# Kernel optimization log

Hardware: AMD Instinct MI355X
Metric: run time of the kernel (lower is better)

Reference implementation:

```python
import jax, jax.numpy as jnp
import numpy as np
import math
from jax import lax

RNN = 256
N_MELS = 80
RF = 5
FRAME = N_MELS * RF  # 400
DYN_CH = 8
DYN_K = 21
STATIC_CH = 8
STATIC_K = 21
PRIOR_LEN = 11


def _betabinom_pmf(n, a, b):
    k = np.arange(n + 1, dtype=np.float64)
    lg = lambda x: np.array([math.lgamma(float(v)) for v in np.atleast_1d(x)])
    logC = lg(n + 1) - lg(k + 1) - lg(n - k + 1)
    logB = lg(k + a) + lg(n - k + b) - lg(np.full_like(k, n + a + b))
    logB0 = math.lgamma(a) + math.lgamma(b) - math.lgamma(a + b)
    return np.exp(logC + logB - logB0)

# prior buffer, flipped as in the torch module (register_buffer('P', ...flip(0)))
PRIOR = jnp.asarray(_betabinom_pmf(PRIOR_LEN - 1, 0.1, 0.9)[::-1].copy(), dtype=jnp.float32)


def gru_cell(x, h, wi, bi, wh, bh):
    # torch GRUCell math
    gi = x @ wi.T + bi
    gh = h @ wh.T + bh
    ir, iz, i_n = jnp.split(gi, 3, axis=-1)
    hr, hz, h_n = jnp.split(gh, 3, axis=-1)
    r = jax.nn.sigmoid(ir + hr)
    z = jax.nn.sigmoid(iz + hz)
    n = jnp.tanh(i_n + r * h_n)
    return (1.0 - z) * n + z * h


def dca(s, alpha, dW_w, dW_b, dV_w, dF_w, dU_w, dT_w, dT_b, dv_w):
    B, S = alpha.shape
    # betabinomial prior: causal conv with flipped pmf
    ap = jnp.pad(alpha, ((0, 0), (PRIOR_LEN - 1, 0)))[:, None, :]  # [B,1,S+10]
    p = lax.conv_general_dilated(ap, PRIOR.reshape(1, 1, -1), (1,), [(0, 0)],
                                 dimension_numbers=('NCH', 'OIH', 'NCH'))[:, 0]  # [B,S]
    p = jnp.log(jnp.clip(p, 1e-6))
    # dynamic filters: one set of 8 kernels per batch element
    G = jnp.tanh(s @ dW_w.T + dW_b) @ dV_w.T  # [B, 8*21]
    g = lax.conv_general_dilated(alpha[None, :, :], G.reshape(B * DYN_CH, 1, DYN_K),
                                 (1,), [((DYN_K - 1) // 2,) * 2],
                                 dimension_numbers=('NCH', 'OIH', 'NCH'),
                                 feature_group_count=B)  # [1, B*8, S]
    g = g.reshape(B, DYN_CH, S).transpose(0, 2, 1)  # [B,S,8]
    # static filters
    f = lax.conv_general_dilated(alpha[:, None, :], dF_w, (1,), [((STATIC_K - 1) // 2,) * 2],
                                 dimension_numbers=('NCH', 'OIH', 'NCH')).transpose(0, 2, 1)  # [B,S,8]
    e = (jnp.tanh(f @ dU_w.T + g @ dT_w.T + dT_b) @ dv_w.T)[..., 0] + p  # [B,S]
    return jax.nn.softmax(e, axis=-1)


def _decode(encoder_outputs, p1_w, p1_b, p2_w, p2_b, a_wi, a_bi, a_wh, a_bh,
            dW_w, dW_b, dV_w, dF_w, dU_w, dT_w, dT_b, dv_w, l_w, l_b,
            g1_wi, g1_bi, g1_wh, g1_bh, g2_wi, g2_bi, g2_wh, g2_bh, pr_w, pr_b, T_dec):
    B, S, _ = encoder_outputs.shape
    frame0 = jnp.zeros((B, FRAME), jnp.float32)
    alpha0 = jnp.zeros((B, S), jnp.float32).at[:, 0].set(1.0)
    ctx0 = jnp.zeros((B, 3 * RNN), jnp.float32)
    h0 = jnp.zeros((B, RNN), jnp.float32)

    def step(carry, _):
        frame, alpha, ctx, h_att, h1, h2 = carry
        # pre-net (eval mode: dropout is identity)
        pre = jax.nn.relu(jax.nn.relu(frame @ p1_w.T + p1_b) @ p2_w.T + p2_b)  # [B,128]
        h_att = gru_cell(jnp.concatenate([ctx, pre], axis=-1), h_att, a_wi, a_bi, a_wh, a_bh)
        alpha = dca(h_att, alpha, dW_w, dW_b, dV_w, dF_w, dU_w, dT_w, dT_b, dv_w)
        ctx = jnp.einsum('bs,bsd->bd', alpha, encoder_outputs)  # [B,768]
        x = jnp.concatenate([ctx, h_att], axis=-1) @ l_w.T + l_b  # [B,256]
        h1 = gru_cell(x, h1, g1_wi, g1_bi, g1_wh, g1_bh)
        x = x + h1
        h2 = gru_cell(x, h2, g2_wi, g2_bi, g2_wh, g2_bh)
        x = x + h2
        out = x @ pr_w.T + pr_b  # [B,400]
        return (out, alpha, ctx, h_att, h1, h2), out

    (_, alphaT, _, _, _, _), outs = lax.scan(step, (frame0, alpha0, ctx0, h0, h0, h0), None, length=T_dec)
    # outs: [T,B,400] -> [B,80,T*5]
    mel = outs.reshape(T_dec, B, N_MELS, RF).transpose(1, 2, 0, 3).reshape(B, N_MELS, T_dec * RF)
    return mel


def setup_inputs() -> dict:
    key = jax.random.key(0)
    ks = iter(jax.random.split(key, 40))
    w = lambda shape: jax.random.normal(next(ks), shape, jnp.float32) * 0.05
    z = lambda shape: jnp.zeros(shape, jnp.float32)
    B, S, D = 64, 512, 768
    return {
        'encoder_outputs': jax.random.normal(next(ks), (B, S, D), jnp.float32),
        'p1_w': w((RNN, FRAME)), 'p1_b': z((RNN,)),
        'p2_w': w((RNN // 2, RNN)), 'p2_b': z((RNN // 2,)),
        'a_wi': w((3 * RNN, 896)), 'a_bi': z((3 * RNN,)), 'a_wh': w((3 * RNN, RNN)), 'a_bh': z((3 * RNN,)),
        'dW_w': w((128, RNN)), 'dW_b': z((128,)),
        'dV_w': w((DYN_CH * DYN_K, 128)),
        'dF_w': w((STATIC_CH, 1, STATIC_K)),
        'dU_w': w((128, STATIC_CH)),
        'dT_w': w((128, DYN_CH)), 'dT_b': z((128,)),
        'dv_w': w((1, 128)),
        'l_w': w((RNN, 4 * RNN)), 'l_b': z((RNN,)),
        'g1_wi': w((3 * RNN, RNN)), 'g1_bi': z((3 * RNN,)), 'g1_wh': w((3 * RNN, RNN)), 'g1_bh': z((3 * RNN,)),
        'g2_wi': w((3 * RNN, RNN)), 'g2_bi': z((3 * RNN,)), 'g2_wh': w((3 * RNN, RNN)), 'g2_bh': z((3 * RNN,)),
        'pr_w': w((FRAME, RNN)), 'pr_b': z((FRAME,)),
        'T_dec': 250,
    }


def reference(encoder_outputs, p1_w, p1_b, p2_w, p2_b, a_wi, a_bi, a_wh, a_bh,
              dW_w, dW_b, dV_w, dF_w, dU_w, dT_w, dT_b, dv_w, l_w, l_b,
              g1_wi, g1_bi, g1_wh, g1_bh, g2_wi, g2_bi, g2_wh, g2_bh, pr_w, pr_b, T_dec):
    return _decode(encoder_outputs, p1_w, p1_b, p2_w, p2_b, a_wi, a_bi, a_wh, a_bh,
                   dW_w, dW_b, dV_w, dF_w, dU_w, dT_w, dT_b, dv_w, l_w, l_b,
                   g1_wi, g1_bi, g1_wh, g1_bh, g2_wi, g2_bi, g2_wh, g2_bh, pr_w, pr_b, T_dec)
```

## Files before the change

kernel.cpp:

```cpp
#include <hip/hip_runtime.h>
#include <cmath>

#define TDEC 250
#define EPS_A 1e-6f

#define NB_GIC  64
#define NB_GA   128
#define NB_WH1  144
#define NB_WH2  152
#define NBLK    160

#define B_CTX(p)  (8192   + (p)*49152)
#define B_HATT(p) (106496 + (p)*16384)
#define B_H1(p)   (139264 + (p)*16384)
#define B_H2(p)   (172032 + (p)*16384)
#define B_GIC(p)  (204800 + (p)*49152)
#define B_GH(p)   (303104 + (p)*49152)
#define B_GH1(p)  (401408 + (p)*49152)
#define B_GH2(p)  (499712 + (p)*49152)
#define ZERO_END  598016
#define CVT_OFF   598016

#define OP1   0u
#define OP2   106496u
#define OAWI  139264u
#define OAWH  827392u
#define ODW   1024000u
#define ODV   1056768u
#define OLW   1078272u
#define OG1I  1340416u
#define OG2I  1537024u
#define OG1H  1733632u
#define OG2H  1930240u
#define OPR   2126848u

struct Prior { float v[11]; };

struct KArgs {
  const float *enc;
  const float *p1w,*p1b,*p2w,*p2b;
  const float *awi,*abi,*awh,*abh;
  const float *dWw,*dWb,*dVw,*dFw,*dUw,*dTw,*dTb,*dvw;
  const float *lw,*lb;
  const float *g1wi,*g1bi,*g1wh,*g1bh;
  const float *g2wi,*g2bi,*g2wh,*g2bh;
  const float *prw,*prb;
  float* ws; float* dout;
  Prior pr;
};

__device__ __forceinline__ float gld(const float* p) {
  return __uint_as_float(__hip_atomic_load((const unsigned*)p, __ATOMIC_RELAXED, __HIP_MEMORY_SCOPE_AGENT));
}
__device__ __forceinline__ void gst(float* p, float v) {
  __hip_atomic_store((unsigned*)p, __float_as_uint(v), __ATOMIC_RELAXED, __HIP_MEMORY_SCOPE_AGENT);
}
__device__ __forceinline__ float sigm(float x) { return 1.f / (1.f + expf(-x)); }

__device__ __forceinline__ float dot8(uint4 w, float4 x0, float4 x1) {
  float a;
  a = __uint_as_float(w.x << 16) * x0.x;
  a = fmaf(__uint_as_float(w.x & 0xffff0000u), x0.y, a);
  a = fmaf(__uint_as_float(w.y << 16),         x0.z, a);
  a = fmaf(__uint_as_float(w.y & 0xffff0000u), x0.w, a);
  a = fmaf(__uint_as_float(w.z << 16),         x1.x, a);
  a = fmaf(__uint_as_float(w.z & 0xffff0000u), x1.y, a);
  a = fmaf(__uint_as_float(w.w << 16),         x1.z, a);
  a = fmaf(__uint_as_float(w.w & 0xffff0000u), x1.w, a);
  return a;
}

__global__ __launch_bounds__(256) void k_init(float* ws) {
  int idx = blockIdx.x * 256 + threadIdx.x;
  for (int i = idx; i < ZERO_END; i += gridDim.x * 256) ws[i] = 0.f;
}

struct CvtSeg { const float* src; unsigned dst; unsigned n; };
struct CvtArgs { CvtSeg s[12]; };
__global__ __launch_bounds__(256) void k_cvt(CvtArgs c, unsigned short* wb) {
  for (unsigned i = blockIdx.x * 256 + threadIdx.x; i < 256u * 416u; i += gridDim.x * 256) {
    unsigned row = i / 416u, col = i - row * 416u;
    unsigned short v = 0;
    if (col < 400u) {
      unsigned u = __float_as_uint(c.s[0].src[row * 400u + col]);
      v = (unsigned short)((u + 0x7fffu + ((u >> 16) & 1u)) >> 16);
    }
    wb[OP1 + i] = v;
  }
  for (int seg = 1; seg < 12; ++seg) {
    const float* s = c.s[seg].src;
    unsigned short* d = wb + c.s[seg].dst;
    unsigned n = c.s[seg].n;
    for (unsigned i = blockIdx.x * 256 + threadIdx.x; i < n; i += gridDim.x * 256) {
      unsigned u = __float_as_uint(s[i]);
      d[i] = (unsigned short)((u + 0x7fffu + ((u >> 16) & 1u)) >> 16);
    }
  }
}

__device__ __forceinline__ void postw(unsigned* fl, int word, unsigned v) {
  asm volatile("s_waitcnt vmcnt(0)" ::: "memory");
  __syncthreads();
  if (threadIdx.x == 0)
    __hip_atomic_store(&fl[blockIdx.x * 32 + word], v, __ATOMIC_RELAXED, __HIP_MEMORY_SCOPE_AGENT);
}
template <int SLP>
__device__ __forceinline__ void pollge(unsigned* fl, int line, int word, unsigned v) {
  while (__hip_atomic_load(&fl[line * 32 + word], __ATOMIC_RELAXED, __HIP_MEMORY_SCOPE_AGENT) < v)
    __builtin_amdgcn_s_sleep(SLP);
}

__global__ __launch_bounds__(1024, 1) void k_decode(KArgs A) {
  __shared__ __align__(16) float sm[16640];
  float* ws = A.ws;
  unsigned* fl = (unsigned*)ws;
  const unsigned short* wb = (const unsigned short*)(ws + CVT_OFF);
  const int blk = blockIdx.x;
  const int tid = threadIdx.x;

  if (blk < 64) {
    const int b = blk, bg = b >> 4;
    float* alpha = sm;
    float* hattl = sm + 512;
    float* h1l   = sm + 768;
    float* h2l   = sm + 1024;
    float* fr    = sm + 1280;
    float* ctxl  = sm + 1696;
    float* xl    = sm + 2464;
    float* x2l   = sm + 2720;
    float* x3l   = sm + 2976;
    float* sal   = sm + 3232;
    float* h1s   = sm + 3776;
    float* pre   = sm + 4032;
    float* sgi   = sm + 4160;
    float* sgh   = sm + 4928;
    float* t1    = sm + 5696;
    float* Gl    = sm + 5824;
    float* sdF   = sm + 6000;
    float* sdU   = sm + 6176;
    float* sdT   = sm + 7200;
    float* sdtb  = sm + 8224;
    float* sdv   = sm + 8352;
    float* es    = sm + 8480;
    float* e     = sm + 9504;
    float* red   = sm + 10016;
    int*   wc    = (int*)(sm + 10032);
    float* lv    = sm + 10040;
    short* li    = (short*)(sm + 10552);

    if (tid < 512) alpha[tid] = (tid == 0) ? 1.f : 0.f;
    if (tid < 256) { hattl[tid] = 0.f; h1l[tid] = 0.f; h2l[tid] = 0.f; }
    if (tid < 416) fr[tid] = 0.f;
    if (tid < 176) sdF[tid] = (tid < 168) ? A.dFw[tid] : 0.f;
    sdU[tid] = A.dUw[tid];
    sdT[tid] = A.dTw[tid];
    if (tid < 128) { sdtb[tid] = A.dTb[tid]; sdv[tid] = A.dvw[tid]; }
    __syncthreads();

    for (int t = 0; t < TDEC; ++t) {
      const int p = t & 1;
      if (tid < 544) { int sg = tid - 10; sal[tid] = (sg >= 0 && sg < 512) ? alpha[sg] : 0.f; }
      __syncthreads();
      {
        int j = tid >> 2, part = tid & 3;
        const uint4* wr = (const uint4*)(wb + OP1 + (size_t)j * 416) + part * 13;
        const float4* xr = (const float4*)fr + part * 26;
        float a = 0.f;
#pragma unroll
        for (int k4 = 0; k4 < 13; ++k4) a += dot8(wr[k4], xr[2*k4], xr[2*k4+1]);
        a += __shfl_xor(a, 1); a += __shfl_xor(a, 2);
        if (part == 0) h1s[j] = fmaxf(a + A.p1b[j], 0.f);
      }
      __syncthreads();
      {
        int j = tid >> 3, part = tid & 7;
        const uint4* wr = (const uint4*)(wb + OP2 + (size_t)j * 256) + part * 4;
        const float4* xr = (const float4*)h1s + part * 8;
        float a = 0.f;
#pragma unroll
        for (int k4 = 0; k4 < 4; ++k4) a += dot8(wr[k4], xr[2*k4], xr[2*k4+1]);
        a += __shfl_xor(a, 1); a += __shfl_xor(a, 2); a += __shfl_xor(a, 4);
        if (part == 0) pre[j] = fmaxf(a + A.p2b[j], 0.f);
      }
      __syncthreads();
      float gipre = 0.f;
      if (tid < 768) {
        const uint4* wr = (const uint4*)(wb + OAWI + (size_t)tid * 896 + 768);
        const float4* xr = (const float4*)pre;
        float a = 0.f;
#pragma unroll
        for (int k4 = 0; k4 < 16; ++k4) a += dot8(wr[k4], xr[2*k4], xr[2*k4+1]);
        gipre = a;
      } else if (tid < 784) {
        pollge<1>(fl, NB_GIC + bg * 16 + (tid - 768), 0, (unsigned)(t + 1));
      } else if (tid < 788) {
        pollge<1>(fl, NB_GA + bg * 4 + (tid - 784), 0, (unsigned)(t + 1));
      }
      __syncthreads();
      if (tid < 768) {
        sgi[tid] = gipre + gld(ws + B_GIC(p) + b * 768 + tid) + A.abi[tid];
        sgh[tid] = gld(ws + B_GH(p) + b * 768 + tid) + A.abh[tid];
      }
      __syncthreads();
      if (tid < 256) {
        float r = sigm(sgi[tid] + sgh[tid]);
        float z = sigm(sgi[256 + tid] + sgh[256 + tid]);
        float n = tanhf(sgi[512 + tid] + r * sgh[512 + tid]);
        float hnew = (1.f - z) * n + z * hattl[tid];
        hattl[tid] = hnew;
        gst(ws + B_HATT(p) + b * 256 + tid, hnew);
      }
      postw(fl, 1, (unsigned)(t + 1));
      {
        int j = tid >> 3, part = tid & 7;
        const uint4* wr = (const uint4*)(wb + ODW + (size_t)j * 256) + part * 4;
        const float4* xr = (const float4*)hattl + part * 8;
        float a = 0.f;
#pragma unroll
        for (int k4 = 0; k4 < 4; ++k4) a += dot8(wr[k4], xr[2*k4], xr[2*k4+1]);
        a += __shfl_xor(a, 1); a += __shfl_xor(a, 2); a += __shfl_xor(a, 4);
        if (part == 0) t1[j] = tanhf(a + A.dWb[j]);
      }
      __syncthreads();
      if (tid < 168) {
        const uint4* wr = (const uint4*)(wb + ODV + (size_t)tid * 128);
        const float4* xr = (const float4*)t1;
        float a = 0.f;
#pragma unroll
        for (int k4 = 0; k4 < 16; ++k4) a += dot8(wr[k4], xr[2*k4], xr[2*k4+1]);
        Gl[tid] = a;
      }
      __syncthreads();
      {
        int sl = tid >> 1, half = tid & 1;
        float f0[8], g0[8];
#pragma unroll
        for (int q = 0; q < 8; ++q) {
          float fa = 0.f, ga = 0.f;
#pragma unroll
          for (int k = 0; k < 21; ++k) {
            float a = sal[sl + k];
            fa = fmaf(sdF[q * 21 + k], a, fa);
            ga = fmaf(Gl[q * 21 + k], a, ga);
          }
          f0[q] = fa; g0[q] = ga;
        }
        float acc = 0.f;
        for (int cc = half * 64; cc < half * 64 + 64; ++cc) {
          float a = sdtb[cc];
#pragma unroll
          for (int q = 0; q < 8; ++q)
            a = fmaf(sdU[cc * 8 + q], f0[q], fmaf(sdT[cc * 8 + q], g0[q], a));
          acc = fmaf(sdv[cc], tanhf(a), acc);
        }
        es[sl * 2 + half] = acc;
      }
      __syncthreads();
      if (tid < 512) {
        float pr = 0.f;
#pragma unroll
        for (int k = 0; k < 11; ++k) pr = fmaf(A.pr.v[k], sal[tid + k], pr);
        e[tid] = es[tid * 2] + es[tid * 2 + 1] + logf(fmaxf(pr, 1e-6f));
      }
      __syncthreads();
      {
        int lane = tid & 63, wv = tid >> 6;
        float e0 = (tid < 512) ? e[tid] : -1e30f;
        float m = e0;
        for (int o = 32; o; o >>= 1) m = fmaxf(m, __shfl_xor(m, o));
        if (lane == 0) red[wv] = m;
        __syncthreads();
        m = red[0];
        for (int w = 1; w < 8; ++w) m = fmaxf(m, red[w]);
        float p0 = (tid < 512) ? expf(e0 - m) : 0.f;
        float s = p0;
        for (int o = 32; o; o >>= 1) s += __shfl_xor(s, o);
        __syncthreads();
        if (lane == 0) red[wv] = s;
        __syncthreads();
        float tot = red[0];
        for (int w = 1; w < 8; ++w) tot += red[w];
        float inv = 1.f / tot;
        float a0 = p0 * inv;
        if (tid < 512) alpha[tid] = a0;
        unsigned long long mk = __ballot(tid < 512 && a0 > EPS_A);
        if (lane == 0 && wv < 8) wc[wv] = (int)__popcll(mk);
        __syncthreads();
        int base = 0;
        for (int w = 0; w < wv && w < 8; ++w) base += wc[w];
        int n = 0;
        for (int w = 0; w < 8; ++w) n += wc[w];
        unsigned long long below = (1ull << lane) - 1ull;
        if (tid < 512 && a0 > EPS_A) {
          int pp = base + (int)__popcll(mk & below);
          li[pp] = (short)tid; lv[pp] = a0;
        }
        __syncthreads();
        const float* encb = A.enc + (size_t)b * 512 * 768;
        if (tid < 768) {
          float acc = 0.f;
          int i = 0;
          for (; i + 4 <= n; i += 4) {
            float v0 = gld(encb + (size_t)li[i] * 768 + tid);
            float v1 = gld(encb + (size_t)li[i+1] * 768 + tid);
            float v2 = gld(encb + (size_t)li[i+2] * 768 + tid);
            float v3 = gld(encb + (size_t)li[i+3] * 768 + tid);
            acc = fmaf(lv[i],v0, fmaf(lv[i+1],v1, fmaf(lv[i+2],v2, fmaf(lv[i+3],v3, acc))));
          }
          for (; i < n; ++i) acc = fmaf(lv[i], gld(encb + (size_t)li[i] * 768 + tid), acc);
          ctxl[tid] = acc;
          gst(ws + B_CTX(p) + b * 768 + tid, acc);
        }
      }
      postw(fl, 0, (unsigned)(t + 1));
      {
        int j = tid >> 2, part = tid & 3;
        const uint4* wr = (const uint4*)(wb + OLW + (size_t)j * 1024) + part * 32;
        const float4* xr = (part < 3) ? ((const float4*)ctxl + part * 64) : (const float4*)hattl;
        float a = 0.f;
#pragma unroll 16
        for (int k4 = 0; k4 < 32; ++k4) a += dot8(wr[k4], xr[2*k4], xr[2*k4+1]);
        a += __shfl_xor(a, 1); a += __shfl_xor(a, 2);
        if (part == 0) xl[j] = a + A.lb[j];
      }
      __syncthreads();
      {
        float giv = 0.f;
        if (tid < 768) {
          const uint4* wr = (const uint4*)(wb + OG1I + (size_t)tid * 256);
          const float4* xr = (const float4*)xl;
          float a = 0.f;
#pragma unroll 16
          for (int k4 = 0; k4 < 32; ++k4) a += dot8(wr[k4], xr[2*k4], xr[2*k4+1]);
          giv = a;
        } else if (tid < 776) {
          pollge<1>(fl, NB_WH1 + (tid - 768), 0, (unsigned)(t + 1));
        }
        __syncthreads();
        if (tid < 768) {
          sgi[tid] = giv + A.g1bi[tid];
          sgh[tid] = gld(ws + B_GH1(p) + b * 768 + tid);
        }
        __syncthreads();
        if (tid < 256) {
          float r = sigm(sgi[tid] + sgh[tid]);
          float z = sigm(sgi[256 + tid] + sgh[256 + tid]);
          float n = tanhf(sgi[512 + tid] + r * sgh[512 + tid]);
          float hnew = (1.f - z) * n + z * h1l[tid];
          h1l[tid] = hnew;
          gst(ws + B_H1(p) + b * 256 + tid, hnew);
          x2l[tid] = xl[tid] + hnew;
        }
        postw(fl, 2, (unsigned)(t + 1));
      }
      {
        float giv = 0.f;
        if (tid < 768) {
          const uint4* wr = (const uint4*)(wb + OG2I + (size_t)tid * 256);
          const float4* xr = (const float4*)x2l;
          float a = 0.f;
#pragma unroll 16
          for (int k4 = 0; k4 < 32; ++k4) a += dot8(wr[k4], xr[2*k4], xr[2*k4+1]);
          giv = a;
        } else if (tid < 776) {
          pollge<1>(fl, NB_WH2 + (tid - 768), 0, (unsigned)(t + 1));
        }
        __syncthreads();
        if (tid < 768) {
          sgi[tid] = giv + A.g2bi[tid];
          sgh[tid] = gld(ws + B_GH2(p) + b * 768 + tid);
        }
        __syncthreads();
        if (tid < 256) {
          float r = sigm(sgi[tid] + sgh[tid]);
          float z = sigm(sgi[256 + tid] + sgh[256 + tid]);
          float n = tanhf(sgi[512 + tid] + r * sgh[512 + tid]);
          float hnew = (1.f - z) * n + z * h2l[tid];
          h2l[tid] = hnew;
          gst(ws + B_H2(p) + b * 256 + tid, hnew);
          x3l[tid] = x2l[tid] + hnew;
        }
        postw(fl, 3, (unsigned)(t + 1));
      }
      if (tid < 800) {
        int j = tid >> 1, part = tid & 1;
        const uint4* wr = (const uint4*)(wb + OPR + (size_t)j * 256) + part * 16;
        const float4* xr = (const float4*)x3l + part * 32;
        float a = 0.f;
#pragma unroll 16
        for (int k4 = 0; k4 < 16; ++k4) a += dot8(wr[k4], xr[2*k4], xr[2*k4+1]);
        a += __shfl_xor(a, 1);
        if (part == 0) {
          float v = a + A.prb[j];
          fr[j] = v;
          gst(A.dout + (size_t)b * 100000 + (j / 5) * 1250 + t * 5 + (j % 5), v);
        }
      }
      __syncthreads();
    }
  } else if (blk < NB_GA) {
    int rb = blk - NB_GIC, bg = rb >> 4, jg = rb & 15;
    int B = bg * 16, R0 = jg * 48;
    float* cl = sm;
    for (int t = 0; t < TDEC; ++t) {
      const int p = t & 1;
      if (tid < 16) pollge<4>(fl, bg * 16 + tid, 0, (unsigned)t);
      __syncthreads();
      for (int idx = tid; idx < 12288; idx += 1024) {
        int bb = idx / 768, k = idx - bb * 768;
        cl[bb * 772 + k] = gld(ws + B_CTX(p ^ 1) + (B + bb) * 768 + k);
      }
      __syncthreads();
      if (tid < 768) {
        int rr = tid >> 4, bb = tid & 15;
        int row = R0 + rr;
        const uint4* wr = (const uint4*)(wb + OAWI + (size_t)row * 896);
        const float4* xr = (const float4*)(cl + bb * 772);
        float a = 0.f;
#pragma unroll 16
        for (int k4 = 0; k4 < 96; ++k4) a += dot8(wr[k4], xr[2*k4], xr[2*k4+1]);
        gst(ws + B_GIC(p) + (B + bb) * 768 + row, a);
      }
      postw(fl, 0, (unsigned)(t + 1));
    }
  } else if (blk < NB_WH1) {
    int rb = blk - NB_GA, bg = rb >> 2, jg = rb & 3;
    int B = bg * 16, R0 = jg * 192;
    float* hl = sm;
    for (int t = 0; t < TDEC; ++t) {
      const int p = t & 1;
      if (tid < 16) pollge<4>(fl, bg * 16 + tid, 1, (unsigned)t);
      __syncthreads();
      for (int idx = tid; idx < 4096; idx += 1024) {
        int bb = idx >> 8, k = idx & 255;
        hl[bb * 260 + k] = gld(ws + B_HATT(p ^ 1) + (B + bb) * 256 + k);
      }
      __syncthreads();
#pragma unroll
      for (int pass = 0; pass < 3; ++pass) {
        int rr = pass * 64 + (tid >> 4), bb = tid & 15;
        int row = R0 + rr;
        const uint4* wr = (const uint4*)(wb + OAWH + (size_t)row * 256);
        const float4* xr = (const float4*)(hl + bb * 260);
        float a = 0.f;
#pragma unroll 16
        for (int k4 = 0; k4 < 32; ++k4) a += dot8(wr[k4], xr[2*k4], xr[2*k4+1]);
        gst(ws + B_GH(p) + (B + bb) * 768 + row, a);
      }
      postw(fl, 0, (unsigned)(t + 1));
    }
  } else {
    const int isW2 = (blk >= NB_WH2);
    const int w = blk - (isW2 ? NB_WH2 : NB_WH1);
    const unsigned OW = isW2 ? OG2H : OG1H;
    const float* bh = isW2 ? A.g2bh : A.g1bh;
    const int hOff0  = isW2 ? B_H2(0)  : B_H1(0);
    const int ghOff0 = isW2 ? B_GH2(0) : B_GH1(0);
    const int word = isW2 ? 3 : 2;
    const int R0 = w * 96;
    float* hl = sm;
    for (int t = 0; t < TDEC; ++t) {
      const int p = t & 1;
      if (tid < 64) pollge<4>(fl, tid, word, (unsigned)t);
      __syncthreads();
      for (int idx = tid; idx < 16384; idx += 1024) {
        int bb = idx >> 8, k = idx & 255;
        hl[bb * 260 + k] = gld(ws + hOff0 + (p ^ 1) * 16384 + bb * 256 + k);
      }
      __syncthreads();
#pragma unroll
      for (int pass = 0; pass < 6; ++pass) {
        int o = pass * 1024 + tid;
        int bb = o & 63, lr = o >> 6;
        int row = R0 + lr;
        const uint4* wr = (const uint4*)(wb + OW + (size_t)row * 256);
        const float4* xr = (const float4*)(hl + bb * 260);
        float a = 0.f;
#pragma unroll 16
        for (int k4 = 0; k4 < 32; ++k4) a += dot8(wr[k4], xr[2*k4], xr[2*k4+1]);
        gst(ws + ghOff0 + p * 49152 + bb * 768 + row, a + bh[row]);
      }
      postw(fl, 0, (unsigned)(t + 1));
    }
  }
}

extern "C" void kernel_launch(void* const* d_in, const int* in_sizes, int n_in,
                              void* d_out, int out_size, void* d_ws, size_t ws_size,
                              hipStream_t stream) {
  (void)in_sizes; (void)n_in; (void)out_size; (void)ws_size;
  KArgs A;
  A.enc  = (const float*)d_in[0];
  A.p1w  = (const float*)d_in[1];  A.p1b  = (const float*)d_in[2];
  A.p2w  = (const float*)d_in[3];  A.p2b  = (const float*)d_in[4];
  A.awi  = (const float*)d_in[5];  A.abi  = (const float*)d_in[6];
  A.awh  = (const float*)d_in[7];  A.abh  = (const float*)d_in[8];
  A.dWw  = (const float*)d_in[9];  A.dWb  = (const float*)d_in[10];
  A.dVw  = (const float*)d_in[11]; A.dFw  = (const float*)d_in[12];
  A.dUw  = (const float*)d_in[13]; A.dTw  = (const float*)d_in[14];
  A.dTb  = (const float*)d_in[15]; A.dvw  = (const float*)d_in[16];
  A.lw   = (const float*)d_in[17]; A.lb   = (const float*)d_in[18];
  A.g1wi = (const float*)d_in[19]; A.g1bi = (const float*)d_in[20];
  A.g1wh = (const float*)d_in[21]; A.g1bh = (const float*)d_in[22];
  A.g2wi = (const float*)d_in[23]; A.g2bi = (const float*)d_in[24];
  A.g2wh = (const float*)d_in[25]; A.g2bh = (const float*)d_in[26];
  A.prw  = (const float*)d_in[27]; A.prb  = (const float*)d_in[28];
  A.ws   = (float*)d_ws;
  A.dout = (float*)d_out;

  {
    double aP = 0.1, bP = 0.9;
    double logB0 = lgamma(aP) + lgamma(bP) - lgamma(aP + bP);
    double pm[11];
    for (int k = 0; k <= 10; ++k) {
      double logC = lgamma(11.0) - lgamma(k + 1.0) - lgamma(11.0 - k);
      double logBt = lgamma(k + aP) + lgamma(10.0 - k + bP) - lgamma(10.0 + aP + bP);
      pm[k] = exp(logC + logBt - logB0);
    }
    for (int k = 0; k < 11; ++k) A.pr.v[k] = (float)pm[10 - k];
  }

  CvtArgs C;
  C.s[0]  = {A.p1w,  OP1,  106496u};
  C.s[1]  = {A.p2w,  OP2,  32768u};
  C.s[2]  = {A.awi,  OAWI, 688128u};
  C.s[3]  = {A.awh,  OAWH, 196608u};
  C.s[4]  = {A.dWw,  ODW,  32768u};
  C.s[5]  = {A.dVw,  ODV,  21504u};
  C.s[6]  = {A.lw,   OLW,  262144u};
  C.s[7]  = {A.g1wi, OG1I, 196608u};
  C.s[8]  = {A.g2wi, OG2I, 196608u};
  C.s[9]  = {A.g1wh, OG1H, 196608u};
  C.s[10] = {A.g2wh, OG2H, 196608u};
  C.s[11] = {A.prw,  OPR,  102400u};

  k_init<<<256, 256, 0, stream>>>((float*)d_ws);
  k_cvt<<<256, 256, 0, stream>>>(C, (unsigned short*)((float*)d_ws + CVT_OFF));
  k_decode<<<NBLK, 1024, 0, stream>>>(A);
}
```

Baseline: 34.81 ms.

## Interleave bf16 weights by k-groups for coalesced per-batch matvec loads

The bf16 weight conversion now writes most per-batch decoder matrices in a k-group-major interleaved layout (8-element chunks, rows contiguous per group), so adjacent threads read adjacent 16-byte chunks. The matvecs are restructured so each thread owns an output row and a slice of K, with partial sums reduced through shared memory instead of wave shuffles. Context and hidden state are also concatenated into one buffer for the linear layer, and the encoder gather switches from atomic loads to plain loads with two accumulators. This adds extra syncthreads and shared-memory reductions per step in exchange for coalesced weight traffic.

```diff
diff --git a/kernel.cpp b/kernel.cpp
--- a/kernel.cpp
+++ b/kernel.cpp
@@ -21,18 +21,19 @@
 #define ZERO_END  598016
 #define CVT_OFF   598016
 
-#define OP1   0u
-#define OP2   106496u
-#define OAWI  139264u
-#define OAWH  827392u
-#define ODW   1024000u
-#define ODV   1056768u
-#define OLW   1078272u
-#define OG1I  1340416u
-#define OG2I  1537024u
-#define OG1H  1733632u
-#define OG2H  1930240u
-#define OPR   2126848u
+#define OP1    0u
+#define OP2    106496u
+#define OAWIP  139264u
+#define ODW    237568u
+#define ODV    270336u
+#define OLW    291840u
+#define OG1I   553984u
+#define OG2I   750592u
+#define OPR    947200u
+#define OAWI   1049600u
+#define OAWH   1737728u
+#define OG1H   1934336u
+#define OG2H   2130944u
 
 struct Prior { float v[11]; };
 
@@ -75,25 +76,26 @@
   for (int i = idx; i < ZERO_END; i += gridDim.x * 256) ws[i] = 0.f;
 }
 
-struct CvtSeg { const float* src; unsigned dst; unsigned n; };
-struct CvtArgs { CvtSeg s[12]; };
+struct CvtSeg { const float* src; unsigned dst; unsigned N, K, KP, sstr, soff, mode; };
+struct CvtArgs { CvtSeg s[13]; };
 __global__ __launch_bounds__(256) void k_cvt(CvtArgs c, unsigned short* wb) {
-  for (unsigned i = blockIdx.x * 256 + threadIdx.x; i < 256u * 416u; i += gridDim.x * 256) {
-    unsigned row = i / 416u, col = i - row * 416u;
-    unsigned short v = 0;
-    if (col < 400u) {
-      unsigned u = __float_as_uint(c.s[0].src[row * 400u + col]);
-      v = (unsigned short)((u + 0x7fffu + ((u >> 16) & 1u)) >> 16);
-    }
-    wb[OP1 + i] = v;
-  }
-  for (int seg = 1; seg < 12; ++seg) {
-    const float* s = c.s[seg].src;
-    unsigned short* d = wb + c.s[seg].dst;
-    unsigned n = c.s[seg].n;
-    for (unsigned i = blockIdx.x * 256 + threadIdx.x; i < n; i += gridDim.x * 256) {
-      unsigned u = __float_as_uint(s[i]);
-      d[i] = (unsigned short)((u + 0x7fffu + ((u >> 16) & 1u)) >> 16);
+  for (int seg = 0; seg < 13; ++seg) {
+    CvtSeg sg = c.s[seg];
+    unsigned short* d = wb + sg.dst;
+    unsigned tot = sg.N * sg.KP;
+    for (unsigned i = blockIdx.x * 256 + threadIdx.x; i < tot; i += gridDim.x * 256) {
+      if (sg.mode == 0) {
+        unsigned u = __float_as_uint(sg.src[i]);
+        d[i] = (unsigned short)((u + 0x7fffu + ((u >> 16) & 1u)) >> 16);
+      } else {
+        unsigned n = i / sg.KP, k = i - n * sg.KP;
+        unsigned short v = 0;
+        if (k < sg.K) {
+          unsigned u = __float_as_uint(sg.src[(size_t)n * sg.sstr + sg.soff + k]);
+          v = (unsigned short)((u + 0x7fffu + ((u >> 16) & 1u)) >> 16);
+        }
+        d[(k >> 3) * (sg.N * 8) + n * 8 + (k & 7)] = v;
+      }
     }
   }
 }
@@ -125,31 +127,32 @@
     float* h1l   = sm + 768;
     float* h2l   = sm + 1024;
     float* fr    = sm + 1280;
-    float* ctxl  = sm + 1696;
-    float* xl    = sm + 2464;
-    float* x2l   = sm + 2720;
-    float* x3l   = sm + 2976;
-    float* sal   = sm + 3232;
-    float* h1s   = sm + 3776;
-    float* pre   = sm + 4032;
-    float* sgi   = sm + 4160;
-    float* sgh   = sm + 4928;
-    float* t1    = sm + 5696;
-    float* Gl    = sm + 5824;
-    float* sdF   = sm + 6000;
-    float* sdU   = sm + 6176;
-    float* sdT   = sm + 7200;
-    float* sdtb  = sm + 8224;
-    float* sdv   = sm + 8352;
-    float* es    = sm + 8480;
-    float* e     = sm + 9504;
-    float* red   = sm + 10016;
-    int*   wc    = (int*)(sm + 10032);
-    float* lv    = sm + 10040;
-    short* li    = (short*)(sm + 10552);
+    float* xcat  = sm + 1696;
+    float* xl    = sm + 2728;
+    float* x2l   = sm + 2984;
+    float* x3l   = sm + 3240;
+    float* sal   = sm + 3496;
+    float* h1s   = sm + 4040;
+    float* pre   = sm + 4296;
+    float* sgi   = sm + 4424;
+    float* sgh   = sm + 5192;
+    float* t1    = sm + 5960;
+    float* Gl    = sm + 6088;
+    float* sdF   = sm + 6264;
+    float* sdU   = sm + 6440;
+    float* sdT   = sm + 7464;
+    float* sdtb  = sm + 8488;
+    float* sdv   = sm + 8616;
+    float* es    = sm + 8744;
+    float* e     = sm + 9768;
+    float* red   = sm + 10280;
+    int*   wc    = (int*)(sm + 10296);
+    float* lv    = sm + 10304;
+    short* li    = (short*)(sm + 10816);
+    float* pt    = sm + 11072;
 
     if (tid < 512) alpha[tid] = (tid == 0) ? 1.f : 0.f;
-    if (tid < 256) { hattl[tid] = 0.f; h1l[tid] = 0.f; h2l[tid] = 0.f; }
+    if (tid < 256) { hattl[tid] = 0.f; h1l[tid] = 0.f; h2l[tid] = 0.f; xcat[768 + tid] = 0.f; }
     if (tid < 416) fr[tid] = 0.f;
     if (tid < 176) sdF[tid] = (tid < 168) ? A.dFw[tid] : 0.f;
     sdU[tid] = A.dUw[tid];
@@ -162,34 +165,49 @@
       if (tid < 544) { int sg = tid - 10; sal[tid] = (sg >= 0 && sg < 512) ? alpha[sg] : 0.f; }
       __syncthreads();
       {
-        int j = tid >> 2, part = tid & 3;
-        const uint4* wr = (const uint4*)(wb + OP1 + (size_t)j * 416) + part * 13;
-        const float4* xr = (const float4*)fr + part * 26;
-        float a = 0.f;
-#pragma unroll
-        for (int k4 = 0; k4 < 13; ++k4) a += dot8(wr[k4], xr[2*k4], xr[2*k4+1]);
-        a += __shfl_xor(a, 1); a += __shfl_xor(a, 2);
-        if (part == 0) h1s[j] = fmaxf(a + A.p1b[j], 0.f);
-      }
-      __syncthreads();
-      {
-        int j = tid >> 3, part = tid & 7;
-        const uint4* wr = (const uint4*)(wb + OP2 + (size_t)j * 256) + part * 4;
-        const float4* xr = (const float4*)h1s + part * 8;
-        float a = 0.f;
-#pragma unroll
-        for (int k4 = 0; k4 < 4; ++k4) a += dot8(wr[k4], xr[2*k4], xr[2*k4+1]);
-        a += __shfl_xor(a, 1); a += __shfl_xor(a, 2); a += __shfl_xor(a, 4);
-        if (part == 0) pre[j] = fmaxf(a + A.p2b[j], 0.f);
+        int part = tid >> 8, j = tid & 255;
+        const float4* xr = (const float4*)fr;
+        float a = 0.f;
+#pragma unroll
+        for (int g = 0; g < 13; ++g) {
+          int gg = part * 13 + g;
+          uint4 w = *(const uint4*)(wb + OP1 + (size_t)gg * 2048 + j * 8);
+          a += dot8(w, xr[gg * 2], xr[gg * 2 + 1]);
+        }
+        pt[part * 260 + j] = a;
+      }
+      __syncthreads();
+      if (tid < 256) h1s[tid] = fmaxf(pt[tid] + pt[260 + tid] + pt[520 + tid] + pt[780 + tid] + A.p1b[tid], 0.f);
+      __syncthreads();
+      {
+        int part = tid >> 7, j = tid & 127;
+        const float4* xr = (const float4*)h1s;
+        float a = 0.f;
+#pragma unroll
+        for (int g = 0; g < 4; ++g) {
+          int gg = part * 4 + g;
+          uint4 w = *(const uint4*)(wb + OP2 + (size_t)gg * 1024 + j * 8);
+          a += dot8(w, xr[gg * 2], xr[gg * 2 + 1]);
+        }
+        pt[part * 132 + j] = a;
+      }
+      __syncthreads();
+      if (tid < 128) {
+        float a = A.p2b[tid];
+#pragma unroll
+        for (int q = 0; q < 8; ++q) a += pt[q * 132 + tid];
+        pre[tid] = fmaxf(a, 0.f);
       }
       __syncthreads();
       float gipre = 0.f;
       if (tid < 768) {
-        const uint4* wr = (const uint4*)(wb + OAWI + (size_t)tid * 896 + 768);
         const float4* xr = (const float4*)pre;
         float a = 0.f;
 #pragma unroll
-        for (int k4 = 0; k4 < 16; ++k4) a += dot8(wr[k4], xr[2*k4], xr[2*k4+1]);
+        for (int g = 0; g < 16; ++g) {
+          uint4 w = *(const uint4*)(wb + OAWIP + (size_t)g * 6144 + tid * 8);
+          a += dot8(w, xr[g * 2], xr[g * 2 + 1]);
+        }
         gipre = a;
       } else if (tid < 784) {
         pollge<1>(fl, NB_GIC + bg * 16 + (tid - 768), 0, (unsigned)(t + 1));
@@ -208,28 +226,44 @@
         float n = tanhf(sgi[512 + tid] + r * sgh[512 + tid]);
         float hnew = (1.f - z) * n + z * hattl[tid];
         hattl[tid] = hnew;
+        xcat[768 + tid] = hnew;
         gst(ws + B_HATT(p) + b * 256 + tid, hnew);
       }
       postw(fl, 1, (unsigned)(t + 1));
       {
-        int j = tid >> 3, part = tid & 7;
-        const uint4* wr = (const uint4*)(wb + ODW + (size_t)j * 256) + part * 4;
-        const float4* xr = (const float4*)hattl + part * 8;
-        float a = 0.f;
-#pragma unroll
-        for (int k4 = 0; k4 < 4; ++k4) a += dot8(wr[k4], xr[2*k4], xr[2*k4+1]);
-        a += __shfl_xor(a, 1); a += __shfl_xor(a, 2); a += __shfl_xor(a, 4);
-        if (part == 0) t1[j] = tanhf(a + A.dWb[j]);
-      }
-      __syncthreads();
-      if (tid < 168) {
-        const uint4* wr = (const uint4*)(wb + ODV + (size_t)tid * 128);
+        int part = tid >> 7, j = tid & 127;
+        const float4* xr = (const float4*)hattl;
+        float a = 0.f;
+#pragma unroll
+        for (int g = 0; g < 4; ++g) {
+          int gg = part * 4 + g;
+          uint4 w = *(const uint4*)(wb + ODW + (size_t)gg * 1024 + j * 8);
+          a += dot8(w, xr[gg * 2], xr[gg * 2 + 1]);
+        }
+        pt[part * 132 + j] = a;
+      }
+      __syncthreads();
+      if (tid < 128) {
+        float a = A.dWb[tid];
+#pragma unroll
+        for (int q = 0; q < 8; ++q) a += pt[q * 132 + tid];
+        t1[tid] = tanhf(a);
+      }
+      __syncthreads();
+      if (tid < 672) {
+        int part = tid / 168, j = tid - part * 168;
         const float4* xr = (const float4*)t1;
         float a = 0.f;
 #pragma unroll
-        for (int k4 = 0; k4 < 16; ++k4) a += dot8(wr[k4], xr[2*k4], xr[2*k4+1]);
-        Gl[tid] = a;
-      }
+        for (int g = 0; g < 4; ++g) {
+          int gg = part * 4 + g;
+          uint4 w = *(const uint4*)(wb + ODV + (size_t)gg * 1344 + j * 8);
+          a += dot8(w, xr[gg * 2], xr[gg * 2 + 1]);
+        }
+        pt[part * 172 + j] = a;
+      }
+      __syncthreads();
+      if (tid < 168) Gl[tid] = pt[tid] + pt[172 + tid] + pt[344 + tid] + pt[516 + tid];
       __syncthreads();
       {
         int sl = tid >> 1, half = tid & 1;
@@ -298,40 +332,50 @@
         __syncthreads();
         const float* encb = A.enc + (size_t)b * 512 * 768;
         if (tid < 768) {
-          float acc = 0.f;
+          float acc0 = 0.f, acc1 = 0.f;
           int i = 0;
-          for (; i + 4 <= n; i += 4) {
-            float v0 = gld(encb + (size_t)li[i] * 768 + tid);
-            float v1 = gld(encb + (size_t)li[i+1] * 768 + tid);
-            float v2 = gld(encb + (size_t)li[i+2] * 768 + tid);
-            float v3 = gld(encb + (size_t)li[i+3] * 768 + tid);
-            acc = fmaf(lv[i],v0, fmaf(lv[i+1],v1, fmaf(lv[i+2],v2, fmaf(lv[i+3],v3, acc))));
+          for (; i + 8 <= n; i += 8) {
+            acc0 = fmaf(lv[i],   encb[(size_t)li[i]   * 768 + tid],
+                   fmaf(lv[i+1], encb[(size_t)li[i+1] * 768 + tid],
+                   fmaf(lv[i+2], encb[(size_t)li[i+2] * 768 + tid],
+                   fmaf(lv[i+3], encb[(size_t)li[i+3] * 768 + tid], acc0))));
+            acc1 = fmaf(lv[i+4], encb[(size_t)li[i+4] * 768 + tid],
+                   fmaf(lv[i+5], encb[(size_t)li[i+5] * 768 + tid],
+                   fmaf(lv[i+6], encb[(size_t)li[i+6] * 768 + tid],
+                   fmaf(lv[i+7], encb[(size_t)li[i+7] * 768 + tid], acc1))));
           }
-          for (; i < n; ++i) acc = fmaf(lv[i], gld(encb + (size_t)li[i] * 768 + tid), acc);
-          ctxl[tid] = acc;
+          for (; i < n; ++i) acc0 = fmaf(lv[i], encb[(size_t)li[i] * 768 + tid], acc0);
+          float acc = acc0 + acc1;
+          xcat[tid] = acc;
           gst(ws + B_CTX(p) + b * 768 + tid, acc);
         }
       }
       postw(fl, 0, (unsigned)(t + 1));
       {
-        int j = tid >> 2, part = tid & 3;
-        const uint4* wr = (const uint4*)(wb + OLW + (size_t)j * 1024) + part * 32;
-        const float4* xr = (part < 3) ? ((const float4*)ctxl + part * 64) : (const float4*)hattl;
+        int part = tid >> 8, j = tid & 255;
+        const float4* xr = (const float4*)xcat;
         float a = 0.f;
 #pragma unroll 16
-        for (int k4 = 0; k4 < 32; ++k4) a += dot8(wr[k4], xr[2*k4], xr[2*k4+1]);
-        a += __shfl_xor(a, 1); a += __shfl_xor(a, 2);
-        if (part == 0) xl[j] = a + A.lb[j];
-      }
+        for (int g = 0; g < 32; ++g) {
+          int gg = part * 32 + g;
+          uint4 w = *(const uint4*)(wb + OLW + (size_t)gg * 2048 + j * 8);
+          a += dot8(w, xr[gg * 2], xr[gg * 2 + 1]);
+        }
+        pt[part * 260 + j] = a;
+      }
+      __syncthreads();
+      if (tid < 256) xl[tid] = pt[tid] + pt[260 + tid] + pt[520 + tid] + pt[780 + tid] + A.lb[tid];
       __syncthreads();
       {
         float giv = 0.f;
         if (tid < 768) {
-          const uint4* wr = (const uint4*)(wb + OG1I + (size_t)tid * 256);
           const float4* xr = (const float4*)xl;
           float a = 0.f;
 #pragma unroll 16
-          for (int k4 = 0; k4 < 32; ++k4) a += dot8(wr[k4], xr[2*k4], xr[2*k4+1]);
+          for (int g = 0; g < 32; ++g) {
+            uint4 w = *(const uint4*)(wb + OG1I + (size_t)g * 6144 + tid * 8);
+            a += dot8(w, xr[g * 2], xr[g * 2 + 1]);
+          }
           giv = a;
         } else if (tid < 776) {
           pollge<1>(fl, NB_WH1 + (tid - 768), 0, (unsigned)(t + 1));
@@ -356,11 +400,13 @@
       {
         float giv = 0.f;
         if (tid < 768) {
-          const uint4* wr = (const uint4*)(wb + OG2I + (size_t)tid * 256);
           const float4* xr = (const float4*)x2l;
           float a = 0.f;
 #pragma unroll 16
-          for (int k4 = 0; k4 < 32; ++k4) a += dot8(wr[k4], xr[2*k4], xr[2*k4+1]);
+          for (int g = 0; g < 32; ++g) {
+            uint4 w = *(const uint4*)(wb + OG2I + (size_t)g * 6144 + tid * 8);
+            a += dot8(w, xr[g * 2], xr[g * 2 + 1]);
+          }
           giv = a;
         } else if (tid < 776) {
           pollge<1>(fl, NB_WH2 + (tid - 768), 0, (unsigned)(t + 1));
@@ -383,18 +429,22 @@
         postw(fl, 3, (unsigned)(t + 1));
       }
       if (tid < 800) {
-        int j = tid >> 1, part = tid & 1;
-        const uint4* wr = (const uint4*)(wb + OPR + (size_t)j * 256) + part * 16;
-        const float4* xr = (const float4*)x3l + part * 32;
-        float a = 0.f;
-#pragma unroll 16
-        for (int k4 = 0; k4 < 16; ++k4) a += dot8(wr[k4], xr[2*k4], xr[2*k4+1]);
-        a += __shfl_xor(a, 1);
-        if (part == 0) {
-          float v = a + A.prb[j];
-          fr[j] = v;
-          gst(A.dout + (size_t)b * 100000 + (j / 5) * 1250 + t * 5 + (j % 5), v);
-        }
+        int part = tid >= 400 ? 1 : 0, j = tid - part * 400;
+        const float4* xr = (const float4*)x3l;
+        float a = 0.f;
+#pragma unroll
+        for (int g = 0; g < 16; ++g) {
+          int gg = part * 16 + g;
+          uint4 w = *(const uint4*)(wb + OPR + (size_t)gg * 3200 + j * 8);
+          a += dot8(w, xr[gg * 2], xr[gg * 2 + 1]);
+        }
+        pt[part * 404 + j] = a;
+      }
+      __syncthreads();
+      if (tid < 400) {
+        float v = pt[tid] + pt[404 + tid] + A.prb[tid];
+        fr[tid] = v;
+        gst(A.dout + (size_t)b * 100000 + (tid / 5) * 1250 + t * 5 + (tid % 5), v);
       }
       __syncthreads();
     }
@@ -521,18 +571,19 @@
   }
 
   CvtArgs C;
-  C.s[0]  = {A.p1w,  OP1,  106496u};
-  C.s[1]  = {A.p2w,  OP2,  32768u};
-  C.s[2]  = {A.awi,  OAWI, 688128u};
-  C.s[3]  = {A.awh,  OAWH, 196608u};
-  C.s[4]  = {A.dWw,  ODW,  32768u};
-  C.s[5]  = {A.dVw,  ODV,  21504u};
-  C.s[6]  = {A.lw,   OLW,  262144u};
-  C.s[7]  = {A.g1wi, OG1I, 196608u};
-  C.s[8]  = {A.g2wi, OG2I, 196608u};
-  C.s[9]  = {A.g1wh, OG1H, 196608u};
-  C.s[10] = {A.g2wh, OG2H, 196608u};
-  C.s[11] = {A.prw,  OPR,  102400u};
+  C.s[0]  = {A.p1w,  OP1,   256, 400, 416, 400, 0, 1};
+  C.s[1]  = {A.p2w,  OP2,   128, 256, 256, 256, 0, 1};
+  C.s[2]  = {A.awi,  OAWIP, 768, 128, 128, 896, 768, 1};
+  C.s[3]  = {A.dWw,  ODW,   128, 256, 256, 256, 0, 1};
+  C.s[4]  = {A.dVw,  ODV,   168, 128, 128, 128, 0, 1};
+  C.s[5]  = {A.lw,   OLW,   256, 1024, 1024, 1024, 0, 1};
+  C.s[6]  = {A.g1wi, OG1I,  768, 256, 256, 256, 0, 1};
+  C.s[7]  = {A.g2wi, OG2I,  768, 256, 256, 256, 0, 1};
+  C.s[8]  = {A.prw,  OPR,   400, 256, 256, 256, 0, 1};
+  C.s[9]  = {A.awi,  OAWI,  768, 896, 896, 896, 0, 0};
+  C.s[10] = {A.awh,  OAWH,  768, 256, 256, 256, 0, 0};
+  C.s[11] = {A.g1wh, OG1H,  768, 256, 256, 256, 0, 0};
+  C.s[12] = {A.g2wh, OG2H,  768, 256, 256, 256, 0, 0};
 
   k_init<<<256, 256, 0, stream>>>((float*)d_ws);
   k_cvt<<<256, 256, 0, stream>>>(C, (unsigned short*)((float*)d_ws + CVT_OFF));
```

Result: faster. 29.67 ms (-14.8%).
